# Performance work log

Hardware: AMD Instinct MI355X
Metric: run time of the kernel (lower is better)

## Reference

```python
import jax, jax.numpy as jnp
import numpy as np

NE = 50000   # num edges (nodes of the line graph)
NA = 800000  # adjacency pairs in the edge graph (~avg degree 16)
NC = 100000  # triadic candidates
F = 64       # edge_feat_dim
H = 128      # hidden_dim
L = 3        # num_layers


def setup_inputs() -> dict:
    key = jax.random.key(0)
    ks = iter(jax.random.split(key, 32))

    def w(shape, scale=0.05):
        return jax.random.normal(next(ks), shape, dtype=jnp.float32) * scale

    inp = {
        "edge_features": jax.random.normal(next(ks), (NE, F), dtype=jnp.float32),
        "adj_dst": jnp.sort(jax.random.randint(next(ks), (NA,), 0, NE)),
        "adj_src": jax.random.randint(next(ks), (NA,), 0, NE),
        "cand_i": jax.random.randint(next(ks), (NC,), 0, NE),
        "cand_j": jax.random.randint(next(ks), (NC,), 0, NE),
        # edge encoder: Linear(F,H) -> ReLU -> Linear(H,H)
        "enc_W1": w((F, H)), "enc_b1": jnp.zeros((H,), jnp.float32),
        "enc_W2": w((H, H)), "enc_b2": jnp.zeros((H,), jnp.float32),
        # per-layer message_net: Linear(2H,H) -> ReLU -> Linear(H,H)
        "msg_W1": w((L, 2 * H, H)), "msg_b1": jnp.zeros((L, H), jnp.float32),
        "msg_W2": w((L, H, H)), "msg_b2": jnp.zeros((L, H), jnp.float32),
        # per-layer update_net: Linear(2H,H) -> ReLU -> Linear(H,H)
        "upd_W1": w((L, 2 * H, H)), "upd_b1": jnp.zeros((L, H), jnp.float32),
        "upd_W2": w((L, H, H)), "upd_b2": jnp.zeros((L, H), jnp.float32),
        # triadic predictor: Linear(2H,H)->ReLU->Linear(H,H)->ReLU->Linear(H,1)
        "pred_W1": w((2 * H, H)), "pred_b1": jnp.zeros((H,), jnp.float32),
        "pred_W2": w((H, H)), "pred_b2": jnp.zeros((H,), jnp.float32),
        "pred_W3": w((H, 1)), "pred_b3": jnp.zeros((1,), jnp.float32),
    }
    return inp


def _mlp2(x, W1, b1, W2, b2):
    return jnp.maximum(x @ W1 + b1, 0.0) @ W2 + b2


def reference(edge_features, adj_dst, adj_src, cand_i, cand_j,
              enc_W1, enc_b1, enc_W2, enc_b2,
              msg_W1, msg_b1, msg_W2, msg_b2,
              upd_W1, upd_b1, upd_W2, upd_b2,
              pred_W1, pred_b1, pred_W2, pred_b2, pred_W3, pred_b3):
    # encode edge features -> [NE, H]
    e = _mlp2(edge_features, enc_W1, enc_b1, enc_W2, enc_b2)

    # degree of each edge-node in the line graph
    deg = jax.ops.segment_sum(jnp.ones((adj_dst.shape[0],), e.dtype), adj_dst,
                              num_segments=NE)  # [NE]
    inv_deg = 1.0 / jnp.maximum(deg, 1.0)
    isolated = (deg == 0.0)[:, None]

    for l in range(L):
        # per-pair message: message_net(concat(e_i, e_j))
        pair = jnp.concatenate([e[adj_dst], e[adj_src]], axis=-1)  # [NA, 2H]
        msgs = _mlp2(pair, msg_W1[l], msg_b1[l], msg_W2[l], msg_b2[l])  # [NA, H]
        agg = jax.ops.segment_sum(msgs, adj_dst, num_segments=NE) * inv_deg[:, None]
        # edges with no neighbors: message_net(concat(e_i, e_i))
        self_msg = _mlp2(jnp.concatenate([e, e], axis=-1),
                         msg_W1[l], msg_b1[l], msg_W2[l], msg_b2[l])
        message = jnp.where(isolated, self_msg, agg)
        # update: update_net(concat(e_i, message_i)), then outer ReLU
        e = _mlp2(jnp.concatenate([e, message], axis=-1),
                  upd_W1[l], upd_b1[l], upd_W2[l], upd_b2[l])
        e = jnp.maximum(e, 0.0)

    # triadic predictor on parent-edge pairs (dropout inactive at eval)
    comb = jnp.concatenate([e[cand_i], e[cand_j]], axis=-1)  # [NC, 2H]
    h = jnp.maximum(comb @ pred_W1 + pred_b1, 0.0)
    h = jnp.maximum(h @ pred_W2 + pred_b2, 0.0)
    logits = (h @ pred_W3 + pred_b3)[:, 0]  # [NC]
    probs = jax.nn.sigmoid(logits)
    return probs, logits
```

## Files before the change

### kernel.cpp

```cpp
#include <hip/hip_runtime.h>
#include <hip/hip_bf16.h>

#define NE 50000
#define NA 800000
#define NC 100000

typedef _Float16 f16;
typedef f16 half8 __attribute__((ext_vector_type(8)));
typedef f16 f16x2 __attribute__((ext_vector_type(2)));
typedef float f32x4 __attribute__((ext_vector_type(4)));

#define OFF_ENC1 0
#define OFF_ENC2 8192
#define OFF_MSGPQ 24576
#define OFF_UPD1 122880
#define OFF_UPD2 221184
#define OFF_PREDPQ 270336
#define OFF_PREDW2 303104
#define TOTAL_WT 319488

#define R_FUSE 49536
#define R_WT 270336
#define R_X 800000
#define R_Z 50000
#define PTOT (R_FUSE + R_WT + R_X + R_Z)

struct KP {
    const float* edge_features;
    const int *adj_dst, *adj_src, *cand_i, *cand_j;
    const float *enc_b1, *enc_b2;
    const float *msg_b1, *msg_W2, *msg_b2;
    const float *upd_W1, *upd_b1, *upd_b2;
    const float *pred_b1, *pred_b2, *pred_W3, *pred_b3;
    f16* wt;
    float* fbias;
    f16 *xb, *eA, *eB, *P0, *Q0, *P1, *Q1;
    int *segStart, *segEnd;
    float *outP, *outL;
    const float* wsrc[20];
    int wK[20], wOff[20], wStr[20], wCum[21];
};


__device__ __forceinline__ void prep_item(const KP& p, int gid) {
    if (gid < R_FUSE) {
        int g = gid >> 7, n = gid & 127;
        int l = g / 129, kk = g % 129;
        const float* U1b = p.upd_W1 + (size_t)l * 32768 + 16384;
        if (kk < 128) {
            const float* w2row = p.msg_W2 + (size_t)l * 16384 + (size_t)kk * 128;
            float s = 0.f;
            for (int m = 0; m < 128; ++m) s += w2row[m] * U1b[m * 128 + n];
            p.wt[OFF_UPD1 + l * 32768 + n * 256 + 128 + kk] = (f16)s;
        } else {
            const float* b2 = p.msg_b2 + l * 128;
            float s = p.upd_b1[l * 128 + n];
            for (int m = 0; m < 128; ++m) s += b2[m] * U1b[m * 128 + n];
            p.fbias[l * 128 + n] = s;
        }
    } else if (gid < R_FUSE + R_WT) {
        int e = gid - R_FUSE;
        int j = 0;
#pragma unroll
        for (int i = 1; i < 20; ++i) j += (e >= p.wCum[i]) ? 1 : 0;
        int r = e - p.wCum[j];
        int K = p.wK[j];
        int k = r % K, n = r / K;
        p.wt[p.wOff[j] + n * p.wStr[j] + k] = (f16)p.wsrc[j][(size_t)k * 128 + n];
    } else if (gid < R_FUSE + R_WT + R_X) {
        int g2 = gid - (R_FUSE + R_WT);
        float4 v = ((const float4*)p.edge_features)[g2];
        f16x2 a = {(f16)v.x, (f16)v.y}, b = {(f16)v.z, (f16)v.w};
        ((f16x2*)p.xb)[g2 * 2] = a;
        ((f16x2*)p.xb)[g2 * 2 + 1] = b;
    } else if (gid < PTOT) {
        int z = gid - (R_FUSE + R_WT + R_X);
        p.segStart[z] = 0;
        p.segEnd[z] = 0;
    }
}

__device__ __forceinline__ void degseg_item(const KP& p, int i) {
    int d = p.adj_dst[i];
    if (i == 0 || p.adj_dst[i - 1] != d) p.segStart[d] = i;
    if (i == NA - 1 || p.adj_dst[i + 1] != d) p.segEnd[d] = i + 1;
}

template <int K1, bool AGG>
__device__ __forceinline__ void do_tile(
    char* SMEM, int tile, const f16* __restrict__ in0,
    const f16* __restrict__ Pin, const f16* __restrict__ Qin,
    const int* __restrict__ adj_src, const int* __restrict__ segStart,
    const int* __restrict__ segEnd,
    const f16* __restrict__ w1t, const int w1s, const float* __restrict__ b1v,
    const f16* __restrict__ w2t, const float* __restrict__ b2v, const bool reluOut,
    f16* __restrict__ oute,
    const f16* __restrict__ wpq, const float* __restrict__ bPp,
    f16* __restrict__ Pout, f16* __restrict__ Qout) {
    constexpr int SA = K1 + 8;
    constexpr int SH = 136;
    f16* Abuf = (f16*)SMEM;
    f16* Hbuf = (f16*)SMEM;
    f16* Ebuf = (f16*)(SMEM + 17408);
    const int t = threadIdx.x, lane = t & 63, wave = t >> 6;
    const int quad = lane >> 4, mn = lane & 15, n0 = wave * 32;
    const int rbase = tile << 6;

    if constexpr (K1 == 64) {
#pragma unroll
        for (int it = 0; it < 2; ++it) {
            int u = it * 256 + t, row = u >> 3, k = (u & 7) * 8, gr = rbase + row;
            half8 v = {};
            if (gr < NE) v = *(const half8*)(in0 + (size_t)gr * 64 + k);
            *(half8*)(Abuf + row * SA + k) = v;
        }
    } else {
#pragma unroll
        for (int it = 0; it < 4; ++it) {
            int u = it * 256 + t, row = u >> 4, k = (u & 15) * 8, gr = rbase + row;
            half8 v = {};
            if (gr < NE) v = *(const half8*)(in0 + (size_t)gr * 128 + k);
            *(half8*)(Abuf + row * SA + k) = v;
        }
    }
    if constexpr (AGG) {
        for (int i = 0; i < 16; ++i) {
            int dst = rbase + wave * 16 + i;
            float a0 = 0.f, a1 = 0.f;
            if (dst < NE) {
                f16x2 p2 = ((const f16x2*)Pin)[(size_t)dst * 64 + lane];
                float pp0 = (float)p2.x, pp1 = (float)p2.y;
                int s = segStart[dst];
                int deg = segEnd[dst] - s;
                if (deg == 0) {
                    f16x2 q2 = ((const f16x2*)Qin)[(size_t)dst * 64 + lane];
                    a0 = fmaxf(pp0 + (float)q2.x, 0.f);
                    a1 = fmaxf(pp1 + (float)q2.y, 0.f);
                } else {
                    float x0 = 0.f, x1 = 0.f;
                    int j = 0;
                    for (; j + 7 < deg; j += 8) {
                        f16x2 q[8];
#pragma unroll
                        for (int u2 = 0; u2 < 8; ++u2)
                            q[u2] = ((const f16x2*)Qin)[(size_t)adj_src[s + j + u2] * 64 + lane];
#pragma unroll
                        for (int u2 = 0; u2 < 8; ++u2) {
                            x0 += fmaxf(pp0 + (float)q[u2].x, 0.f);
                            x1 += fmaxf(pp1 + (float)q[u2].y, 0.f);
                        }
                    }
                    for (; j < deg; ++j) {
                        f16x2 q2 = ((const f16x2*)Qin)[(size_t)adj_src[s + j] * 64 + lane];
                        x0 += fmaxf(pp0 + (float)q2.x, 0.f);
                        x1 += fmaxf(pp1 + (float)q2.y, 0.f);
                    }
                    float sc = 1.f / (float)deg;
                    a0 = x0 * sc;
                    a1 = x1 * sc;
                }
            }
            f16x2 o = {(f16)a0, (f16)a1};
            *(f16x2*)(Abuf + (wave * 16 + i) * SA + 128 + lane * 2) = o;
        }
    }
    __syncthreads();

    f32x4 acc[4][2];
    {
        float bb0 = b1v[n0 + mn], bb1 = b1v[n0 + 16 + mn];
#pragma unroll
        for (int mt = 0; mt < 4; ++mt) {
            acc[mt][0] = (f32x4){bb0, bb0, bb0, bb0};
            acc[mt][1] = (f32x4){bb1, bb1, bb1, bb1};
        }
    }
#pragma unroll
    for (int kc = 0; kc < K1 / 32; ++kc) {
        half8 wA = *(const half8*)(w1t + (size_t)(n0 + mn) * w1s + kc * 32 + quad * 8);
        half8 wB = *(const half8*)(w1t + (size_t)(n0 + 16 + mn) * w1s + kc * 32 + quad * 8);
        half8 af[4];
#pragma unroll
        for (int mt = 0; mt < 4; ++mt)
            af[mt] = *(const half8*)(Abuf + (mt * 16 + mn) * SA + kc * 32 + quad * 8);
#pragma unroll
        for (int mt = 0; mt < 4; ++mt) {
            acc[mt][0] = __builtin_amdgcn_mfma_f32_16x16x32_f16(af[mt], wA, acc[mt][0], 0, 0, 0);
            acc[mt][1] = __builtin_amdgcn_mfma_f32_16x16x32_f16(af[mt], wB, acc[mt][1], 0, 0, 0);
        }
    }
    __syncthreads();
#pragma unroll
    for (int mt = 0; mt < 4; ++mt)
#pragma unroll
        for (int nt = 0; nt < 2; ++nt)
#pragma unroll
            for (int r = 0; r < 4; ++r)
                Hbuf[(mt * 16 + quad * 4 + r) * SH + n0 + nt * 16 + mn] =
                    (f16)fmaxf(acc[mt][nt][r], 0.f);
    __syncthreads();

    {
        float bb0 = b2v[n0 + mn], bb1 = b2v[n0 + 16 + mn];
#pragma unroll
        for (int mt = 0; mt < 4; ++mt) {
            acc[mt][0] = (f32x4){bb0, bb0, bb0, bb0};
            acc[mt][1] = (f32x4){bb1, bb1, bb1, bb1};
        }
    }
#pragma unroll
    for (int kc = 0; kc < 4; ++kc) {
        half8 wA = *(const half8*)(w2t + (size_t)(n0 + mn) * 128 + kc * 32 + quad * 8);
        half8 wB = *(const half8*)(w2t + (size_t)(n0 + 16 + mn) * 128 + kc * 32 + quad * 8);
        half8 af[4];
#pragma unroll
        for (int mt = 0; mt < 4; ++mt)
            af[mt] = *(const half8*)(Hbuf + (mt * 16 + mn) * SH + kc * 32 + quad * 8);
#pragma unroll
        for (int mt = 0; mt < 4; ++mt) {
            acc[mt][0] = __builtin_amdgcn_mfma_f32_16x16x32_f16(af[mt], wA, acc[mt][0], 0, 0, 0);
            acc[mt][1] = __builtin_amdgcn_mfma_f32_16x16x32_f16(af[mt], wB, acc[mt][1], 0, 0, 0);
        }
    }
#pragma unroll
    for (int mt = 0; mt < 4; ++mt)
#pragma unroll
        for (int nt = 0; nt < 2; ++nt)
#pragma unroll
            for (int r = 0; r < 4; ++r) {
                float v = acc[mt][nt][r];
                if (reluOut) v = fmaxf(v, 0.f);
                Ebuf[(mt * 16 + quad * 4 + r) * SH + n0 + nt * 16 + mn] = (f16)v;
            }
    __syncthreads();

#pragma unroll
    for (int it = 0; it < 4; ++it) {
        int u = it * 256 + t, row = u >> 4, k = (u & 15) * 8, gr = rbase + row;
        if (gr < NE) {
            half8 v = *(const half8*)(Ebuf + row * SH + k);
            *(half8*)(oute + (size_t)gr * 128 + k) = v;
        }
    }

    {
        float bb0 = bPp[n0 + mn], bb1 = bPp[n0 + 16 + mn];
#pragma unroll
        for (int mt = 0; mt < 4; ++mt) {
            acc[mt][0] = (f32x4){bb0, bb0, bb0, bb0};
            acc[mt][1] = (f32x4){bb1, bb1, bb1, bb1};
        }
    }
#pragma unroll
    for (int kc = 0; kc < 4; ++kc) {
        half8 wA = *(const half8*)(wpq + (size_t)(n0 + mn) * 128 + kc * 32 + quad * 8);
        half8 wB = *(const half8*)(wpq + (size_t)(n0 + 16 + mn) * 128 + kc * 32 + quad * 8);
        half8 af[4];
#pragma unroll
        for (int mt = 0; mt < 4; ++mt)
            af[mt] = *(const half8*)(Ebuf + (mt * 16 + mn) * SH + kc * 32 + quad * 8);
#pragma unroll
        for (int mt = 0; mt < 4; ++mt) {
            acc[mt][0] = __builtin_amdgcn_mfma_f32_16x16x32_f16(af[mt], wA, acc[mt][0], 0, 0, 0);
            acc[mt][1] = __builtin_amdgcn_mfma_f32_16x16x32_f16(af[mt], wB, acc[mt][1], 0, 0, 0);
        }
    }
#pragma unroll
    for (int mt = 0; mt < 4; ++mt)
#pragma unroll
        for (int nt = 0; nt < 2; ++nt)
#pragma unroll
            for (int r = 0; r < 4; ++r) {
                int gr = rbase + mt * 16 + quad * 4 + r;
                if (gr < NE)
                    Pout[(size_t)gr * 128 + n0 + nt * 16 + mn] = (f16)acc[mt][nt][r];
            }
#pragma unroll
    for (int mt = 0; mt < 4; ++mt) {
        acc[mt][0] = (f32x4){0.f, 0.f, 0.f, 0.f};
        acc[mt][1] = (f32x4){0.f, 0.f, 0.f, 0.f};
    }
#pragma unroll
    for (int kc = 0; kc < 4; ++kc) {
        half8 wA = *(const half8*)(wpq + 16384 + (size_t)(n0 + mn) * 128 + kc * 32 + quad * 8);
        half8 wB = *(const half8*)(wpq + 16384 + (size_t)(n0 + 16 + mn) * 128 + kc * 32 + quad * 8);
        half8 af[4];
#pragma unroll
        for (int mt = 0; mt < 4; ++mt)
            af[mt] = *(const half8*)(Ebuf + (mt * 16 + mn) * SH + kc * 32 + quad * 8);
#pragma unroll
        for (int mt = 0; mt < 4; ++mt) {
            acc[mt][0] = __builtin_amdgcn_mfma_f32_16x16x32_f16(af[mt], wA, acc[mt][0], 0, 0, 0);
            acc[mt][1] = __builtin_amdgcn_mfma_f32_16x16x32_f16(af[mt], wB, acc[mt][1], 0, 0, 0);
        }
    }
#pragma unroll
    for (int mt = 0; mt < 4; ++mt)
#pragma unroll
        for (int nt = 0; nt < 2; ++nt)
#pragma unroll
            for (int r = 0; r < 4; ++r) {
                int gr = rbase + mt * 16 + quad * 4 + r;
                if (gr < NE)
                    Qout[(size_t)gr * 128 + n0 + nt * 16 + mn] = (f16)acc[mt][nt][r];
            }
}

__device__ __forceinline__ void pred_tile(const KP& p, char* SMEM, float* w3s,
                                          float* psum, int tile, float b3v) {
    constexpr int SA = 136, SO = 133;
    f16* Abuf = (f16*)SMEM;
    float* Obuf = (float*)SMEM;
    const int t = threadIdx.x, lane = t & 63, wave = t >> 6;
    const int quad = lane >> 4, mn = lane & 15, n0 = wave * 32;
    const int rbase = tile << 6;
#pragma unroll
    for (int it = 0; it < 4; ++it) {
        int u = it * 256 + t, row = u >> 4, k = (u & 15) * 8, gr = rbase + row;
        half8 v = {};
        if (gr < NC) {
            int ii = p.cand_i[gr], jj = p.cand_j[gr];
            half8 a = *(const half8*)(p.P1 + (size_t)ii * 128 + k);
            half8 b = *(const half8*)(p.Q1 + (size_t)jj * 128 + k);
#pragma unroll
            for (int x = 0; x < 8; ++x)
                v[x] = (f16)fmaxf((float)a[x] + (float)b[x], 0.f);
        }
        *(half8*)(Abuf + row * SA + k) = v;
    }
    __syncthreads();
    f32x4 acc[4][2];
    {
        float bb0 = p.pred_b2[n0 + mn], bb1 = p.pred_b2[n0 + 16 + mn];
#pragma unroll
        for (int mt = 0; mt < 4; ++mt) {
            acc[mt][0] = (f32x4){bb0, bb0, bb0, bb0};
            acc[mt][1] = (f32x4){bb1, bb1, bb1, bb1};
        }
    }
#pragma unroll
    for (int kc = 0; kc < 4; ++kc) {
        half8 wA = *(const half8*)(p.wt + OFF_PREDW2 + (size_t)(n0 + mn) * 128 + kc * 32 + quad * 8);
        half8 wB = *(const half8*)(p.wt + OFF_PREDW2 + (size_t)(n0 + 16 + mn) * 128 + kc * 32 + quad * 8);
        half8 af[4];
#pragma unroll
        for (int mt = 0; mt < 4; ++mt)
            af[mt] = *(const half8*)(Abuf + (mt * 16 + mn) * SA + kc * 32 + quad * 8);
#pragma unroll
        for (int mt = 0; mt < 4; ++mt) {
            acc[mt][0] = __builtin_amdgcn_mfma_f32_16x16x32_f16(af[mt], wA, acc[mt][0], 0, 0, 0);
            acc[mt][1] = __builtin_amdgcn_mfma_f32_16x16x32_f16(af[mt], wB, acc[mt][1], 0, 0, 0);
        }
    }
    __syncthreads();
#pragma unroll
    for (int mt = 0; mt < 4; ++mt)
#pragma unroll
        for (int nt = 0; nt < 2; ++nt)
#pragma unroll
            for (int r = 0; r < 4; ++r)
                Obuf[(mt * 16 + quad * 4 + r) * SO + n0 + nt * 16 + mn] =
                    fmaxf(acc[mt][nt][r], 0.f);
    __syncthreads();
    {
        int row = t & 63, q4 = t >> 6;
        float s = 0.f;
#pragma unroll
        for (int i = 0; i < 32; ++i)
            s += Obuf[row * SO + q4 * 32 + i] * w3s[q4 * 32 + i];
        psum[t] = s;
    }
    __syncthreads();
    if (t < 64) {
        int gr = rbase + t;
        if (gr < NC) {
            float lg = psum[t] + psum[t + 64] + psum[t + 128] + psum[t + 192] + b3v;
            p.outL[gr] = lg;
            p.outP[gr] = 1.f / (1.f + expf(-lg));
        }
    }
}

__device__ __forceinline__ void upd_layer_ptrs(const KP& p, int l,
    const f16*& ein, f16*& eout, const f16*& Pin, const f16*& Qin,
    f16*& Pout, f16*& Qout, const f16*& wpq, const float*& bP) {
    ein = (l & 1) ? p.eB : p.eA;
    eout = (l & 1) ? p.eA : p.eB;
    Pin = (l & 1) ? p.P1 : p.P0;
    Qin = (l & 1) ? p.Q1 : p.Q0;
    Pout = (l & 1) ? p.P0 : p.P1;
    Qout = (l & 1) ? p.Q0 : p.Q1;
    wpq = (l < 2) ? (p.wt + OFF_MSGPQ + (l + 1) * 32768) : (p.wt + OFF_PREDPQ);
    bP = (l < 2) ? (p.msg_b1 + (l + 1) * 128) : p.pred_b1;
}

__global__ void k_prep(KP p) {
    int gid = blockIdx.x * 256 + threadIdx.x;
    if (gid < PTOT) prep_item(p, gid);
}
__global__ __launch_bounds__(256, 4) void k_encdeg(KP p) {
    __shared__ __align__(16) char SMEM[34816];
    do_tile<64, false>(SMEM, blockIdx.x, p.xb, nullptr, nullptr, nullptr, nullptr, nullptr,
                       p.wt + OFF_ENC1, 64, p.enc_b1, p.wt + OFF_ENC2, p.enc_b2, false,
                       p.eA, p.wt + OFF_MSGPQ, p.msg_b1, p.P0, p.Q0);
    const int nthr = gridDim.x * 256;
    for (int i = blockIdx.x * 256 + threadIdx.x; i < NA; i += nthr) degseg_item(p, i);
}
__global__ __launch_bounds__(256, 4) void k_upd(KP p, int l) {
    __shared__ __align__(16) char SMEM[34816];
    const f16 *ein, *Pin, *Qin, *wpq;
    f16 *eout, *Pout, *Qout;
    const float* bP;
    upd_layer_ptrs(p, l, ein, eout, Pin, Qin, Pout, Qout, wpq, bP);
    do_tile<256, true>(SMEM, blockIdx.x, ein, Pin, Qin, p.adj_src, p.segStart, p.segEnd,
                       p.wt + OFF_UPD1 + l * 32768, 256, p.fbias + l * 128,
                       p.wt + OFF_UPD2 + l * 16384, p.upd_b2 + l * 128, true,
                       eout, wpq, bP, Pout, Qout);
}
__global__ __launch_bounds__(256, 4) void k_pred(KP p) {
    __shared__ __align__(16) char SMEM[34816];
    __shared__ float w3s[128];
    __shared__ float psum[256];
    if (threadIdx.x < 128) w3s[threadIdx.x] = p.pred_W3[threadIdx.x];
    float b3v = p.pred_b3[0];
    pred_tile(p, SMEM, w3s, psum, blockIdx.x, b3v);
}

extern "C" void kernel_launch(void* const* d_in, const int* in_sizes, int n_in,
                              void* d_out, int out_size, void* d_ws, size_t ws_size,
                              hipStream_t stream) {
    KP p;
    p.edge_features = (const float*)d_in[0];
    p.adj_dst = (const int*)d_in[1];
    p.adj_src = (const int*)d_in[2];
    p.cand_i = (const int*)d_in[3];
    p.cand_j = (const int*)d_in[4];
    const float* enc_W1 = (const float*)d_in[5];
    p.enc_b1 = (const float*)d_in[6];
    const float* enc_W2 = (const float*)d_in[7];
    p.enc_b2 = (const float*)d_in[8];
    const float* msg_W1 = (const float*)d_in[9];
    p.msg_b1 = (const float*)d_in[10];
    p.msg_W2 = (const float*)d_in[11];
    p.msg_b2 = (const float*)d_in[12];
    p.upd_W1 = (const float*)d_in[13];
    p.upd_b1 = (const float*)d_in[14];
    const float* upd_W2 = (const float*)d_in[15];
    p.upd_b2 = (const float*)d_in[16];
    const float* pred_W1 = (const float*)d_in[17];
    p.pred_b1 = (const float*)d_in[18];
    const float* pred_W2 = (const float*)d_in[19];
    p.pred_b2 = (const float*)d_in[20];
    p.pred_W3 = (const float*)d_in[21];
    p.pred_b3 = (const float*)d_in[22];

    char* ws = (char*)d_ws;
    size_t off = 0;
    auto alloc = [&](size_t bytes) -> void* {
        void* q = ws + off;
        off = (off + bytes + 255) & ~(size_t)255;
        return q;
    };
    p.wt = (f16*)alloc((size_t)TOTAL_WT * 2);
    p.fbias = (float*)alloc(3 * 128 * 4);
    p.xb = (f16*)alloc((size_t)NE * 64 * 2);
    p.eA = (f16*)alloc((size_t)NE * 128 * 2);
    p.eB = (f16*)alloc((size_t)NE * 128 * 2);
    p.P0 = (f16*)alloc((size_t)NE * 128 * 2);
    p.Q0 = (f16*)alloc((size_t)NE * 128 * 2);
    p.P1 = (f16*)alloc((size_t)NE * 128 * 2);
    p.Q1 = (f16*)alloc((size_t)NE * 128 * 2);
    p.segStart = (int*)alloc((size_t)NE * 4);
    p.segEnd = (int*)alloc((size_t)NE * 4);
    p.outP = (float*)d_out;
    p.outL = (float*)d_out + NC;

    int idx = 0, c = 0;
    auto addj = [&](const float* s, int K, int o, int st) {
        p.wsrc[idx] = s; p.wK[idx] = K; p.wOff[idx] = o;
        p.wStr[idx] = st; p.wCum[idx] = c;
        c += K * 128; idx++;
    };
    addj(enc_W1, 64, OFF_ENC1, 64);
    addj(enc_W2, 128, OFF_ENC2, 128);
    for (int l = 0; l < 3; ++l) addj(msg_W1 + (size_t)l * 32768, 128, OFF_MSGPQ + l * 32768, 128);
    for (int l = 0; l < 3; ++l) addj(msg_W1 + (size_t)l * 32768 + 16384, 128, OFF_MSGPQ + l * 32768 + 16384, 128);
    for (int l = 0; l < 3; ++l) addj(p.upd_W1 + (size_t)l * 32768, 128, OFF_UPD1 + l * 32768, 256);
    for (int l = 0; l < 3; ++l) addj(upd_W2 + (size_t)l * 16384, 128, OFF_UPD2 + l * 16384, 128);
    addj(pred_W1, 128, OFF_PREDPQ, 128);
    addj(pred_W1 + 16384, 128, OFF_PREDPQ + 16384, 128);
    addj(pred_W2, 128, OFF_PREDW2, 128);
    for (int i = idx; i <= 20; ++i) p.wCum[i] = c;

    const int tilesNE = (NE + 63) / 64;
    const int tilesNC = (NC + 63) / 64;
    k_prep<<<(PTOT + 255) / 256, 256, 0, stream>>>(p);
    k_encdeg<<<tilesNE, 256, 0, stream>>>(p);
    for (int l = 0; l < 3; ++l) k_upd<<<tilesNE, 256, 0, stream>>>(p, l);
    k_pred<<<tilesNC, 256, 0, stream>>>(p);

    (void)in_sizes; (void)n_in; (void)out_size; (void)ws_size;
}
```

Before: 438.6 us.

## Vectorize neighbor aggregation with 16-byte gathers across four rows per wave

Restructures the gather-aggregate loop so each lane loads 8 contiguous f16 values (half8) of a neighbor row instead of 2, with a wave handling four destination rows at a time (16 lanes per row). The isolated-node case is folded into the same loop by using the node itself as the single neighbor. This cuts the number of memory instructions and raises bytes per request for the irregular Q gathers. Launch bounds are loosened from 4 to 2 blocks per SIMD minimum, giving the compiler more registers for the wider loads at a possible cost in occupancy.

```diff
diff --git a/kernel.cpp b/kernel.cpp
--- a/kernel.cpp
+++ b/kernel.cpp
@@ -124,44 +124,55 @@
         }
     }
     if constexpr (AGG) {
-        for (int i = 0; i < 16; ++i) {
-            int dst = rbase + wave * 16 + i;
-            float a0 = 0.f, a1 = 0.f;
-            if (dst < NE) {
-                f16x2 p2 = ((const f16x2*)Pin)[(size_t)dst * 64 + lane];
-                float pp0 = (float)p2.x, pp1 = (float)p2.y;
-                int s = segStart[dst];
-                int deg = segEnd[dst] - s;
-                if (deg == 0) {
-                    f16x2 q2 = ((const f16x2*)Qin)[(size_t)dst * 64 + lane];
-                    a0 = fmaxf(pp0 + (float)q2.x, 0.f);
-                    a1 = fmaxf(pp1 + (float)q2.y, 0.f);
-                } else {
-                    float x0 = 0.f, x1 = 0.f;
-                    int j = 0;
-                    for (; j + 7 < deg; j += 8) {
-                        f16x2 q[8];
-#pragma unroll
-                        for (int u2 = 0; u2 < 8; ++u2)
-                            q[u2] = ((const f16x2*)Qin)[(size_t)adj_src[s + j + u2] * 64 + lane];
-#pragma unroll
-                        for (int u2 = 0; u2 < 8; ++u2) {
-                            x0 += fmaxf(pp0 + (float)q[u2].x, 0.f);
-                            x1 += fmaxf(pp1 + (float)q[u2].y, 0.f);
-                        }
+        const int cl = mn;
+#pragma unroll
+        for (int g = 0; g < 4; ++g) {
+            int drow = wave * 16 + g * 4 + quad;
+            int dst = rbase + drow;
+            bool ok = dst < NE;
+            int s = 0, deg = 0;
+            if (ok) {
+                s = segStart[dst];
+                deg = segEnd[dst] - s;
+            }
+            bool iso = (deg == 0);
+            int d1 = iso ? 1 : deg;
+            half8 pv = {};
+            if (ok) pv = *(const half8*)(Pin + (size_t)dst * 128 + cl * 8);
+            float x[8] = {0.f, 0.f, 0.f, 0.f, 0.f, 0.f, 0.f, 0.f};
+            if (ok) {
+                int j = 0;
+                for (; j + 3 < d1; j += 4) {
+                    int s0 = adj_src[s + j];
+                    int s1 = adj_src[s + j + 1];
+                    int s2 = adj_src[s + j + 2];
+                    int s3 = adj_src[s + j + 3];
+                    half8 q0 = *(const half8*)(Qin + (size_t)s0 * 128 + cl * 8);
+                    half8 q1 = *(const half8*)(Qin + (size_t)s1 * 128 + cl * 8);
+                    half8 q2 = *(const half8*)(Qin + (size_t)s2 * 128 + cl * 8);
+                    half8 q3 = *(const half8*)(Qin + (size_t)s3 * 128 + cl * 8);
+#pragma unroll
+                    for (int c2 = 0; c2 < 8; ++c2) {
+                        float pc = (float)pv[c2];
+                        x[c2] += fmaxf(pc + (float)q0[c2], 0.f) +
+                                 fmaxf(pc + (float)q1[c2], 0.f) +
+                                 fmaxf(pc + (float)q2[c2], 0.f) +
+                                 fmaxf(pc + (float)q3[c2], 0.f);
                     }
-                    for (; j < deg; ++j) {
-                        f16x2 q2 = ((const f16x2*)Qin)[(size_t)adj_src[s + j] * 64 + lane];
-                        x0 += fmaxf(pp0 + (float)q2.x, 0.f);
-                        x1 += fmaxf(pp1 + (float)q2.y, 0.f);
-                    }
-                    float sc = 1.f / (float)deg;
-                    a0 = x0 * sc;
-                    a1 = x1 * sc;
                 }
+                for (; j < d1; ++j) {
+                    int sj = iso ? dst : adj_src[s + j];
+                    half8 qj = *(const half8*)(Qin + (size_t)sj * 128 + cl * 8);
+#pragma unroll
+                    for (int c2 = 0; c2 < 8; ++c2)
+                        x[c2] += fmaxf((float)pv[c2] + (float)qj[c2], 0.f);
+                }
+                float sc = 1.f / (float)d1;
+                half8 o;
+#pragma unroll
+                for (int c2 = 0; c2 < 8; ++c2) o[c2] = (f16)(x[c2] * sc);
+                *(half8*)(Abuf + drow * SA + 128 + cl * 8) = o;
             }
-            f16x2 o = {(f16)a0, (f16)a1};
-            *(f16x2*)(Abuf + (wave * 16 + i) * SA + 128 + lane * 2) = o;
         }
     }
     __syncthreads();
@@ -398,7 +409,7 @@
     int gid = blockIdx.x * 256 + threadIdx.x;
     if (gid < PTOT) prep_item(p, gid);
 }
-__global__ __launch_bounds__(256, 4) void k_encdeg(KP p) {
+__global__ __launch_bounds__(256, 2) void k_encdeg(KP p) {
     __shared__ __align__(16) char SMEM[34816];
     do_tile<64, false>(SMEM, blockIdx.x, p.xb, nullptr, nullptr, nullptr, nullptr, nullptr,
                        p.wt + OFF_ENC1, 64, p.enc_b1, p.wt + OFF_ENC2, p.enc_b2, false,
@@ -406,7 +417,7 @@
     const int nthr = gridDim.x * 256;
     for (int i = blockIdx.x * 256 + threadIdx.x; i < NA; i += nthr) degseg_item(p, i);
 }
-__global__ __launch_bounds__(256, 4) void k_upd(KP p, int l) {
+__global__ __launch_bounds__(256, 2) void k_upd(KP p, int l) {
     __shared__ __align__(16) char SMEM[34816];
     const f16 *ein, *Pin, *Qin, *wpq;
     f16 *eout, *Pout, *Qout;
@@ -417,7 +428,7 @@
                        p.wt + OFF_UPD2 + l * 16384, p.upd_b2 + l * 128, true,
                        eout, wpq, bP, Pout, Qout);
 }
-__global__ __launch_bounds__(256, 4) void k_pred(KP p) {
+__global__ __launch_bounds__(256, 2) void k_pred(KP p) {
     __shared__ __align__(16) char SMEM[34816];
     __shared__ float w3s[128];
     __shared__ float psum[256];
```

Measured after the change: 392.5 us. 1.12x faster.
